# Kernel tuning notes

Hardware: AMD Instinct MI355X
Metric: run time of the kernel (lower is better)

The kernel has to match this reference:

```python
import jax, jax.numpy as jnp
import numpy as np

B, L, NUM_AA, E, H = 128, 2048, 20, 16, 128

def _mlp(x, W1, b1, W2, b2, W3, b3):
    h = jax.nn.relu(x @ W1 + b1)
    h = jax.nn.relu(h @ W2 + b2)
    return h @ W3 + b3

def _mlp_params(key, in_dim):
    k1, k2, k3 = jax.random.split(key, 3)
    W1 = jax.random.normal(k1, (in_dim, H), jnp.float32) / np.sqrt(in_dim)
    W2 = jax.random.normal(k2, (H, H), jnp.float32) / np.sqrt(H)
    W3 = jax.random.normal(k3, (H, 1), jnp.float32) / np.sqrt(H)
    return W1, jnp.zeros((H,), jnp.float32), W2, jnp.zeros((H,), jnp.float32), W3, jnp.zeros((1,), jnp.float32)

def setup_inputs() -> dict:
    key = jax.random.key(0)
    kR, ks, ke, kl, kt, kp = jax.random.split(key, 6)
    inp = {
        'R': jax.random.normal(kR, (B, L, 3), jnp.float32) * 3.8,  # ~CA-CA scale
        'seq': jax.random.randint(ks, (B, L), 0, NUM_AA),
        'emb': jax.random.normal(ke, (NUM_AA, E), jnp.float32),
    }
    for pref, k, d in (('fl', kl, 1 + 2 * E), ('ft', kt, 1 + 3 * E), ('fp', kp, 2 + 4 * E)):
        W1, b1, W2, b2, W3, b3 = _mlp_params(k, d)
        inp.update({f'{pref}_W1': W1, f'{pref}_b1': b1, f'{pref}_W2': W2, f'{pref}_b2': b2, f'{pref}_W3': W3, f'{pref}_b3': b3})
    return inp

def _energy(R, e, fl, ft, fp):
    d = R[:, 1:, :] - R[:, :-1, :]                      # [B,L-1,3] bond vectors
    lengths = jnp.linalg.norm(d, axis=-1)               # [B,L-1]
    x_l = jnp.concatenate([lengths[..., None], e[:, :-1, :], e[:, 1:, :]], axis=-1)
    E_l = _mlp(x_l, *fl)[..., 0].sum(axis=1)
    # bond angles at atom i+1 between (R[i]-R[i+1]) and (R[i+2]-R[i+1])
    u, v = -d[:, :-1, :], d[:, 1:, :]                   # [B,L-2,3]
    cos_t = jnp.sum(u * v, axis=-1) / (jnp.linalg.norm(u, axis=-1) * jnp.linalg.norm(v, axis=-1))
    theta_in = jnp.clip(cos_t, -1.0, 1.0)               # use_cos_theta=True -> cos(arccos(clip))
    x_t = jnp.concatenate([theta_in[..., None], e[:, :-2, :], e[:, 1:-1, :], e[:, 2:, :]], axis=-1)
    E_t = _mlp(x_t, *ft)[..., 0].sum(axis=1)
    # torsions over quadruples
    b1, b2, b3 = d[:, :-2, :], d[:, 1:-1, :], d[:, 2:, :]
    n1 = jnp.cross(b1, b2)
    n2 = jnp.cross(b2, b3)
    b2u = b2 / jnp.linalg.norm(b2, axis=-1, keepdims=True)
    m1 = jnp.cross(n1, b2u)
    phi = jnp.arctan2(jnp.sum(m1 * n2, axis=-1), jnp.sum(n1 * n2, axis=-1))  # [B,L-3]
    sc = jnp.stack([jnp.sin(phi), jnp.cos(phi)], axis=-1)                    # [B,L-3,2]
    x_p = jnp.concatenate([sc, e[:, :-3, :], e[:, 1:-2, :], e[:, 2:-1, :], e[:, 3:, :]], axis=-1)
    E_p = _mlp(x_p, *fp)[..., 0].sum(axis=1)
    return E_l + E_t + E_p

def reference(R, seq, emb,
              fl_W1, fl_b1, fl_W2, fl_b2, fl_W3, fl_b3,
              ft_W1, ft_b1, ft_W2, ft_b2, ft_W3, ft_b3,
              fp_W1, fp_b1, fp_W2, fp_b2, fp_W3, fp_b3):
    e = emb[seq]                                        # [B,L,E]
    return _energy(R, e,
                   (fl_W1, fl_b1, fl_W2, fl_b2, fl_W3, fl_b3),
                   (ft_W1, ft_b1, ft_W2, ft_b2, ft_W3, ft_b3),
                   (fp_W1, fp_b1, fp_W2, fp_b2, fp_W3, fp_b3))
```

## Files before the change

### kernel.cpp

```cpp
#include <hip/hip_runtime.h>


typedef short bf16x8 __attribute__((ext_vector_type(8)));
typedef float f32x4  __attribute__((ext_vector_type(4)));

constexpr int Lc  = 2048;
constexpr int SHs = 136;

union FragU { uint4 u; bf16x8 v; };

__device__ __forceinline__ unsigned short f2bf(float f) {
    union { float f; unsigned u; } v; v.f = f;
    unsigned u = v.u;
    u = u + 0x7FFFu + ((u >> 16) & 1u);
    return (unsigned short)(u >> 16);
}

__device__ __forceinline__ unsigned pkbf(float a, float b) {
    unsigned ua = __float_as_uint(a) + 0x8000u;
    unsigned ub = __float_as_uint(b) + 0x8000u;
    return __builtin_amdgcn_perm(ub, ua, 0x07060302u);
}

__global__ __launch_bounds__(256)
void prep_kernel(const float* __restrict__ W1_0, const float* __restrict__ b1_0,
                 const float* __restrict__ W1_1, const float* __restrict__ b1_1,
                 const float* __restrict__ W1_2, const float* __restrict__ b1_2,
                 const float* __restrict__ W2_0, const float* __restrict__ W2_1,
                 const float* __restrict__ W2_2,
                 const float* __restrict__ emb, char* __restrict__ ws,
                 float* __restrict__ out)
{
    const int tid = blockIdx.x * 256 + threadIdx.x;
    const int np  = gridDim.x * 256;
    if (blockIdx.x == 0 && threadIdx.x < 128) out[threadIdx.x] = 0.0f;

    unsigned short* d2 = (unsigned short*)ws;
    for (int o = tid; o < 3 * 16384; o += np) {
        int t = o >> 14, r = o & 16383, col = r >> 7, k = r & 127;
        const float* W2 = (t == 0) ? W2_0 : (t == 1) ? W2_1 : W2_2;
        d2[o] = f2bf(W2[k * 128 + col]);
    }
    unsigned short* d1 = (unsigned short*)(ws + 98304);
    for (int o = tid; o < 3 * 12288; o += np) {
        int t = o / 12288, r = o - t * 12288, hid = r / 96, k = r - hid * 96;
        const int NE16 = (t == 0) ? 32 : (t == 1) ? 48 : 64;
        const int NG   = (t == 2) ? 2 : 1;
        const float* W1 = (t == 0) ? W1_0 : (t == 1) ? W1_1 : W1_2;
        const float* b1 = (t == 0) ? b1_0 : (t == 1) ? b1_1 : b1_2;
        float v = 0.0f;
        if (k >= 16) {
            int j = k - 16;
            if (j < NE16) v = W1[(NG + j) * 128 + hid];
        } else if (k == 4) v = b1[hid];
        else if (t == 0 && k == 0) v = W1_0[hid];
        else if (t == 1 && k == 1) v = W1_1[hid];
        else if (t == 2 && k == 2) v = W1_2[hid];
        else if (t == 2 && k == 3) v = W1_2[128 + hid];
        d1[o] = f2bf(v);
    }
    unsigned short* eb = (unsigned short*)(ws + 172032);
    for (int i = tid; i < 320; i += np) eb[i] = f2bf(emb[i]);
}

struct SMem {
    unsigned short H1s[128 * SHs];
    float  Rbuf[393];
    uint2  geomh[128];
    int    seqb[132];
    unsigned short ebuf[320];
    float  part[4];
};

template<int TYPE>
__device__ __forceinline__ void type_pass(
    SMem& sm, const char* __restrict__ ws,
    const float* __restrict__ b2, const float* __restrict__ w3,
    int i0, int wv, int q, int c, f32x4& p4)
{
    constexpr int NEMB  = (TYPE == 0) ? 2 : (TYPE == 1) ? 3 : 4;
    constexpr int KS    = (TYPE == 2) ? 3 : 2;
    constexpr int ROWSB = Lc - 1 - TYPE;

    const unsigned short* w1t = (const unsigned short*)(ws + 98304 + TYPE * 24576);
    const unsigned short* w2t = (const unsigned short*)(ws + TYPE * 32768);
    const f32x4 z4 = (f32x4){0.f, 0.f, 0.f, 0.f};

    FragU A1[2][3];
#pragma unroll
    for (int mt = 0; mt < 2; ++mt)
#pragma unroll
        for (int ks = 0; ks < KS; ++ks)
            A1[mt][ks].u = *(const uint4*)&w1t[(wv * 32 + mt * 16 + c) * 96 + ks * 32 + q * 8];

#pragma unroll
    for (int h = 0; h < 2; ++h) {
        f32x4 acc1[2][4];
#pragma unroll
        for (int mt = 0; mt < 2; ++mt)
#pragma unroll
            for (int nt = 0; nt < 4; ++nt)
                acc1[mt][nt] = z4;

#pragma unroll
        for (int ks = 0; ks < KS; ++ks) {
            const int k0 = ks * 32 + q * 8;
            const int j = (k0 - 16) >> 4, off = (k0 - 16) & 15;
#pragma unroll
            for (int nt = 0; nt < 4; ++nt) {
                const int m = h * 64 + nt * 16 + c;
                FragU bb;
                if (ks == 0 && q == 0) {
                    uint2 g = sm.geomh[m];
                    bb.u = make_uint4(g.x, g.y, 0x00003F80u, 0u);
                } else if (k0 >= 16 && j < NEMB) {
                    bb.u = *(const uint4*)&sm.ebuf[sm.seqb[m + j] * 16 + off];
                } else {
                    bb.u = make_uint4(0u, 0u, 0u, 0u);
                }
                acc1[0][nt] = __builtin_amdgcn_mfma_f32_16x16x32_bf16(A1[0][ks].v, bb.v, acc1[0][nt], 0, 0, 0);
                acc1[1][nt] = __builtin_amdgcn_mfma_f32_16x16x32_bf16(A1[1][ks].v, bb.v, acc1[1][nt], 0, 0, 0);
            }
        }

#pragma unroll
        for (int mt = 0; mt < 2; ++mt)
#pragma unroll
            for (int nt = 0; nt < 4; ++nt) {
                f32x4 v = __builtin_elementwise_max(acc1[mt][nt], z4);
                uint2 pk;
                pk.x = pkbf(v[0], v[1]);
                pk.y = pkbf(v[2], v[3]);
                *(uint2*)&sm.H1s[(h * 64 + nt * 16 + c) * SHs + wv * 32 + mt * 16 + q * 4] = pk;
            }
    }

    FragU B2[2][4];
#pragma unroll
    for (int nt = 0; nt < 2; ++nt)
#pragma unroll
        for (int ks = 0; ks < 4; ++ks)
            B2[nt][ks].u = *(const uint4*)&w2t[(wv * 32 + nt * 16 + c) * 128 + ks * 32 + q * 8];
    float b2v[2], w3v[2];
#pragma unroll
    for (int nt = 0; nt < 2; ++nt) {
        int col2 = wv * 32 + nt * 16 + c;
        b2v[nt] = b2[col2]; w3v[nt] = w3[col2];
    }
    __syncthreads();

#pragma unroll
    for (int h = 0; h < 2; ++h) {
        f32x4 acc2[4][2];
#pragma unroll
        for (int mt = 0; mt < 4; ++mt)
#pragma unroll
            for (int nt = 0; nt < 2; ++nt)
                acc2[mt][nt] = z4;
#pragma unroll
        for (int ks2 = 0; ks2 < 4; ++ks2)
#pragma unroll
            for (int mt = 0; mt < 4; ++mt) {
                bf16x8 aa = *(const bf16x8*)&sm.H1s[(h * 64 + mt * 16 + c) * SHs + ks2 * 32 + q * 8];
                acc2[mt][0] = __builtin_amdgcn_mfma_f32_16x16x32_bf16(aa, B2[0][ks2].v, acc2[mt][0], 0, 0, 0);
                acc2[mt][1] = __builtin_amdgcn_mfma_f32_16x16x32_bf16(aa, B2[1][ks2].v, acc2[mt][1], 0, 0, 0);
            }

#pragma unroll
        for (int mt = 0; mt < 4; ++mt) {
            int mbase = h * 64 + mt * 16 + q * 4;
            if (i0 + mbase + 3 < ROWSB) {
#pragma unroll
                for (int nt = 0; nt < 2; ++nt) {
                    f32x4 v = acc2[mt][nt] + b2v[nt];
                    v = __builtin_elementwise_max(v, z4);
                    p4 += v * w3v[nt];
                }
            } else {
#pragma unroll
                for (int rg = 0; rg < 4; ++rg)
                    if (i0 + mbase + rg < ROWSB) {
                        p4[rg] += fmaxf(acc2[mt][0][rg] + b2v[0], 0.f) * w3v[0];
                        p4[rg] += fmaxf(acc2[mt][1][rg] + b2v[1], 0.f) * w3v[1];
                    }
            }
        }
    }
    __syncthreads();
}

__global__ __launch_bounds__(256, 4)
void energy_kernel(const float* __restrict__ R, const int* __restrict__ seq,
                   const char* __restrict__ ws,
                   const float* b2_0, const float* b2_1, const float* b2_2,
                   const float* w3_0, const float* w3_1, const float* w3_2,
                   const float* b3_0, const float* b3_1, const float* b3_2,
                   float* __restrict__ out)
{
    __shared__ SMem sm;
    const int tid = threadIdx.x;
    const int b   = blockIdx.y;
    const int i0  = blockIdx.x * 128;
    const int lane = tid & 63, wv = tid >> 6;
    const int q = lane >> 4, c = lane & 15;

    for (int t = tid; t < 393; t += 256) {
        int lr = t / 3, comp = t - lr * 3;
        int row = min(i0 + lr, Lc - 1);
        sm.Rbuf[t] = R[((size_t)b * Lc + row) * 3 + comp];
    }
    for (int t = tid; t < 131; t += 256)
        sm.seqb[t] = seq[b * Lc + min(i0 + t, Lc - 1)];
    {
        const uint4* se = (const uint4*)(ws + 172032);
        for (int t = tid; t < 40; t += 256) ((uint4*)sm.ebuf)[t] = se[t];
    }
    __syncthreads();

    if (tid < 128) {
        const float* p0 = &sm.Rbuf[tid * 3];
        float ax = p0[3] - p0[0], ay = p0[4] - p0[1], az = p0[5] - p0[2];
        float bx = p0[6] - p0[3], by = p0[7] - p0[4], bz = p0[8] - p0[5];
        float cx = p0[9] - p0[6], cy = p0[10] - p0[7], cz = p0[11] - p0[8];
        float na2 = ax * ax + ay * ay + az * az;
        float len = sqrtf(na2);
        float nb2 = bx * bx + by * by + bz * bz;
        float duv = -(ax * bx + ay * by + az * bz);
        float cost = fminf(fmaxf(duv / sqrtf(na2 * nb2), -1.0f), 1.0f);
        float n1x = ay * bz - az * by, n1y = az * bx - ax * bz, n1z = ax * by - ay * bx;
        float n2x = by * cz - bz * cy, n2y = bz * cx - bx * cz, n2z = bx * cy - by * cx;
        float binv = 1.0f / sqrtf(nb2);
        float ux = bx * binv, uy = by * binv, uz = bz * binv;
        float m1x = n1y * uz - n1z * uy, m1y = n1z * ux - n1x * uz, m1z = n1x * uy - n1y * ux;
        float yv = m1x * n2x + m1y * n2y + m1z * n2z;
        float xv = n1x * n2x + n1y * n2y + n1z * n2z;
        float inv = 1.0f / sqrtf(xv * xv + yv * yv);
        sm.geomh[tid] = make_uint2(pkbf(len, cost), pkbf(yv * inv, xv * inv));
    }
    __syncthreads();

    f32x4 p4 = (f32x4){0.f, 0.f, 0.f, 0.f};
    type_pass<0>(sm, ws, b2_0, w3_0, i0, wv, q, c, p4);
    type_pass<1>(sm, ws, b2_1, w3_1, i0, wv, q, c, p4);
    type_pass<2>(sm, ws, b2_2, w3_2, i0, wv, q, c, p4);

    float p = p4[0] + p4[1] + p4[2] + p4[3];
#pragma unroll
    for (int off = 32; off > 0; off >>= 1)
        p += __shfl_down(p, off);
    if (lane == 0) sm.part[wv] = p;
    __syncthreads();
    if (tid == 0) {
        float tot = sm.part[0] + sm.part[1] + sm.part[2] + sm.part[3];
        tot += b3_0[0] * (float)min(Lc - 1 - i0, 128);
        tot += b3_1[0] * (float)min(Lc - 2 - i0, 128);
        tot += b3_2[0] * (float)min(Lc - 3 - i0, 128);
        atomicAdd(&out[b], tot);
    }
}

extern "C" void kernel_launch(void* const* d_in, const int* in_sizes, int n_in,
                              void* d_out, int out_size, void* d_ws, size_t ws_size,
                              hipStream_t stream) {
    const float* R   = (const float*)d_in[0];
    const int*   seq = (const int*)d_in[1];
    const float* emb = (const float*)d_in[2];
    float* out = (float*)d_out;
    char*  ws  = (char*)d_ws;

    prep_kernel<<<dim3(96), dim3(256), 0, stream>>>(
        (const float*)d_in[3],  (const float*)d_in[4],
        (const float*)d_in[9],  (const float*)d_in[10],
        (const float*)d_in[15], (const float*)d_in[16],
        (const float*)d_in[5],  (const float*)d_in[11], (const float*)d_in[17],
        emb, ws, out);

    dim3 grid(16, 128), block(256);
    energy_kernel<<<grid, block, 0, stream>>>(
        R, seq, ws,
        (const float*)d_in[6],  (const float*)d_in[12], (const float*)d_in[18],
        (const float*)d_in[7],  (const float*)d_in[13], (const float*)d_in[19],
        (const float*)d_in[8],  (const float*)d_in[14], (const float*)d_in[20],
        out);
}
```

Before: 159.4 us.

## Switch MLP matmuls from 16x16x32 to 32x32x16 bf16 MFMA tiles

```diff
diff --git a/kernel.cpp b/kernel.cpp
--- a/kernel.cpp
+++ b/kernel.cpp
@@ -1,8 +1,9 @@
 #include <hip/hip_runtime.h>
 
 
-typedef short bf16x8 __attribute__((ext_vector_type(8)));
-typedef float f32x4  __attribute__((ext_vector_type(4)));
+typedef short bf16x8  __attribute__((ext_vector_type(8)));
+typedef float f32x4   __attribute__((ext_vector_type(4)));
+typedef float f32x16  __attribute__((ext_vector_type(16)));
 
 constexpr int Lc  = 2048;
 constexpr int SHs = 136;
@@ -76,113 +77,102 @@
 __device__ __forceinline__ void type_pass(
     SMem& sm, const char* __restrict__ ws,
     const float* __restrict__ b2, const float* __restrict__ w3,
-    int i0, int wv, int q, int c, f32x4& p4)
+    int i0, int wv, int ln31, int hi, f32x4& p4)
 {
     constexpr int NEMB  = (TYPE == 0) ? 2 : (TYPE == 1) ? 3 : 4;
-    constexpr int KS    = (TYPE == 2) ? 3 : 2;
+    constexpr int STEPS = 1 + NEMB;
     constexpr int ROWSB = Lc - 1 - TYPE;
 
     const unsigned short* w1t = (const unsigned short*)(ws + 98304 + TYPE * 24576);
     const unsigned short* w2t = (const unsigned short*)(ws + TYPE * 32768);
     const f32x4 z4 = (f32x4){0.f, 0.f, 0.f, 0.f};
 
-    FragU A1[2][3];
-#pragma unroll
-    for (int mt = 0; mt < 2; ++mt)
-#pragma unroll
-        for (int ks = 0; ks < KS; ++ks)
-            A1[mt][ks].u = *(const uint4*)&w1t[(wv * 32 + mt * 16 + c) * 96 + ks * 32 + q * 8];
+    FragU A1[STEPS];
+#pragma unroll
+    for (int s = 0; s < STEPS; ++s)
+        A1[s].u = *(const uint4*)&w1t[(wv * 32 + ln31) * 96 + s * 16 + hi * 8];
 
 #pragma unroll
     for (int h = 0; h < 2; ++h) {
-        f32x4 acc1[2][4];
-#pragma unroll
-        for (int mt = 0; mt < 2; ++mt)
-#pragma unroll
-            for (int nt = 0; nt < 4; ++nt)
-                acc1[mt][nt] = z4;
-
-#pragma unroll
-        for (int ks = 0; ks < KS; ++ks) {
-            const int k0 = ks * 32 + q * 8;
-            const int j = (k0 - 16) >> 4, off = (k0 - 16) & 15;
-#pragma unroll
-            for (int nt = 0; nt < 4; ++nt) {
-                const int m = h * 64 + nt * 16 + c;
+        f32x16 acc1[2];
+        acc1[0] = (f32x16)(0.f);
+        acc1[1] = (f32x16)(0.f);
+
+#pragma unroll
+        for (int s = 0; s < STEPS; ++s) {
+#pragma unroll
+            for (int rt = 0; rt < 2; ++rt) {
+                const int row = h * 64 + rt * 32 + ln31;
                 FragU bb;
-                if (ks == 0 && q == 0) {
-                    uint2 g = sm.geomh[m];
-                    bb.u = make_uint4(g.x, g.y, 0x00003F80u, 0u);
-                } else if (k0 >= 16 && j < NEMB) {
-                    bb.u = *(const uint4*)&sm.ebuf[sm.seqb[m + j] * 16 + off];
+                if (s == 0) {
+                    if (hi == 0) {
+                        uint2 g = sm.geomh[row];
+                        bb.u = make_uint4(g.x, g.y, 0x00003F80u, 0u);
+                    } else {
+                        bb.u = make_uint4(0u, 0u, 0u, 0u);
+                    }
                 } else {
-                    bb.u = make_uint4(0u, 0u, 0u, 0u);
+                    bb.u = *(const uint4*)&sm.ebuf[sm.seqb[row + (s - 1)] * 16 + hi * 8];
                 }
-                acc1[0][nt] = __builtin_amdgcn_mfma_f32_16x16x32_bf16(A1[0][ks].v, bb.v, acc1[0][nt], 0, 0, 0);
-                acc1[1][nt] = __builtin_amdgcn_mfma_f32_16x16x32_bf16(A1[1][ks].v, bb.v, acc1[1][nt], 0, 0, 0);
+                acc1[rt] = __builtin_amdgcn_mfma_f32_32x32x16_bf16(A1[s].v, bb.v, acc1[rt], 0, 0, 0);
             }
         }
 
 #pragma unroll
-        for (int mt = 0; mt < 2; ++mt)
-#pragma unroll
-            for (int nt = 0; nt < 4; ++nt) {
-                f32x4 v = __builtin_elementwise_max(acc1[mt][nt], z4);
+        for (int rt = 0; rt < 2; ++rt) {
+            const int row = h * 64 + rt * 32 + ln31;
+#pragma unroll
+            for (int g = 0; g < 4; ++g) {
+                float v0 = fmaxf(acc1[rt][4 * g + 0], 0.f);
+                float v1 = fmaxf(acc1[rt][4 * g + 1], 0.f);
+                float v2 = fmaxf(acc1[rt][4 * g + 2], 0.f);
+                float v3 = fmaxf(acc1[rt][4 * g + 3], 0.f);
                 uint2 pk;
-                pk.x = pkbf(v[0], v[1]);
-                pk.y = pkbf(v[2], v[3]);
-                *(uint2*)&sm.H1s[(h * 64 + nt * 16 + c) * SHs + wv * 32 + mt * 16 + q * 4] = pk;
-            }
-    }
-
-    FragU B2[2][4];
-#pragma unroll
-    for (int nt = 0; nt < 2; ++nt)
-#pragma unroll
-        for (int ks = 0; ks < 4; ++ks)
-            B2[nt][ks].u = *(const uint4*)&w2t[(wv * 32 + nt * 16 + c) * 128 + ks * 32 + q * 8];
-    float b2v[2], w3v[2];
-#pragma unroll
-    for (int nt = 0; nt < 2; ++nt) {
-        int col2 = wv * 32 + nt * 16 + c;
-        b2v[nt] = b2[col2]; w3v[nt] = w3[col2];
-    }
+                pk.x = pkbf(v0, v1);
+                pk.y = pkbf(v2, v3);
+                *(uint2*)&sm.H1s[row * SHs + wv * 32 + 8 * g + 4 * hi] = pk;
+            }
+        }
+    }
+
+    FragU B2[8];
+#pragma unroll
+    for (int s2 = 0; s2 < 8; ++s2)
+        B2[s2].u = *(const uint4*)&w2t[(wv * 32 + ln31) * 128 + s2 * 16 + hi * 8];
+    const float b2v = b2[wv * 32 + ln31];
+    const float w3v = w3[wv * 32 + ln31];
     __syncthreads();
 
 #pragma unroll
     for (int h = 0; h < 2; ++h) {
-        f32x4 acc2[4][2];
-#pragma unroll
-        for (int mt = 0; mt < 4; ++mt)
-#pragma unroll
-            for (int nt = 0; nt < 2; ++nt)
-                acc2[mt][nt] = z4;
-#pragma unroll
-        for (int ks2 = 0; ks2 < 4; ++ks2)
-#pragma unroll
-            for (int mt = 0; mt < 4; ++mt) {
-                bf16x8 aa = *(const bf16x8*)&sm.H1s[(h * 64 + mt * 16 + c) * SHs + ks2 * 32 + q * 8];
-                acc2[mt][0] = __builtin_amdgcn_mfma_f32_16x16x32_bf16(aa, B2[0][ks2].v, acc2[mt][0], 0, 0, 0);
-                acc2[mt][1] = __builtin_amdgcn_mfma_f32_16x16x32_bf16(aa, B2[1][ks2].v, acc2[mt][1], 0, 0, 0);
-            }
-
-#pragma unroll
-        for (int mt = 0; mt < 4; ++mt) {
-            int mbase = h * 64 + mt * 16 + q * 4;
-            if (i0 + mbase + 3 < ROWSB) {
-#pragma unroll
-                for (int nt = 0; nt < 2; ++nt) {
-                    f32x4 v = acc2[mt][nt] + b2v[nt];
-                    v = __builtin_elementwise_max(v, z4);
-                    p4 += v * w3v[nt];
+        f32x16 acc2[2];
+        acc2[0] = (f32x16)(0.f);
+        acc2[1] = (f32x16)(0.f);
+#pragma unroll
+        for (int s2 = 0; s2 < 8; ++s2)
+#pragma unroll
+            for (int rt = 0; rt < 2; ++rt) {
+                const int row = h * 64 + rt * 32 + ln31;
+                bf16x8 aa = *(const bf16x8*)&sm.H1s[row * SHs + s2 * 16 + hi * 8];
+                acc2[rt] = __builtin_amdgcn_mfma_f32_32x32x16_bf16(aa, B2[s2].v, acc2[rt], 0, 0, 0);
+            }
+
+#pragma unroll
+        for (int rt = 0; rt < 2; ++rt) {
+#pragma unroll
+            for (int g = 0; g < 4; ++g) {
+                const int rbase = i0 + h * 64 + rt * 32 + 8 * g + 4 * hi;
+                f32x4 v;
+                v[0] = acc2[rt][4 * g + 0]; v[1] = acc2[rt][4 * g + 1];
+                v[2] = acc2[rt][4 * g + 2]; v[3] = acc2[rt][4 * g + 3];
+                v = __builtin_elementwise_max(v + b2v, z4);
+                if (rbase + 3 < ROWSB) {
+                    p4 += v * w3v;
+                } else {
+#pragma unroll
+                    for (int rg = 0; rg < 4; ++rg)
+                        if (rbase + rg < ROWSB) p4[rg] += v[rg] * w3v;
                 }
-            } else {
-#pragma unroll
-                for (int rg = 0; rg < 4; ++rg)
-                    if (i0 + mbase + rg < ROWSB) {
-                        p4[rg] += fmaxf(acc2[mt][0][rg] + b2v[0], 0.f) * w3v[0];
-                        p4[rg] += fmaxf(acc2[mt][1][rg] + b2v[1], 0.f) * w3v[1];
-                    }
             }
         }
     }
@@ -202,7 +192,7 @@
     const int b   = blockIdx.y;
     const int i0  = blockIdx.x * 128;
     const int lane = tid & 63, wv = tid >> 6;
-    const int q = lane >> 4, c = lane & 15;
+    const int ln31 = lane & 31, hi = lane >> 5;
 
     for (int t = tid; t < 393; t += 256) {
         int lr = t / 3, comp = t - lr * 3;
@@ -240,9 +230,9 @@
     __syncthreads();
 
     f32x4 p4 = (f32x4){0.f, 0.f, 0.f, 0.f};
-    type_pass<0>(sm, ws, b2_0, w3_0, i0, wv, q, c, p4);
-    type_pass<1>(sm, ws, b2_1, w3_1, i0, wv, q, c, p4);
-    type_pass<2>(sm, ws, b2_2, w3_2, i0, wv, q, c, p4);
+    type_pass<0>(sm, ws, b2_0, w3_0, i0, wv, ln31, hi, p4);
+    type_pass<1>(sm, ws, b2_1, w3_1, i0, wv, ln31, hi, p4);
+    type_pass<2>(sm, ws, b2_2, w3_2, i0, wv, ln31, hi, p4);
 
     float p = p4[0] + p4[1] + p4[2] + p4[3];
 #pragma unroll
```

New measurement: 154.4 us. 3.1% less time.
